# Kernel tuning notes

Hardware: AMD Instinct MI355X
Metric: run time of the kernel (lower is better)

The kernel has to match this reference:

```python
import jax, jax.numpy as jnp
import numpy as np

N_EMBED = 384
HEAD_SIZE = 64
B, T = 512, 256


def setup_inputs() -> dict:
    key = jax.random.key(0)
    kx, kq, kk, kv = jax.random.split(key, 4)
    x = jax.random.normal(kx, (B, T, N_EMBED), dtype=jnp.float32)
    # nn.Linear(n_embed, head_size, bias=False): y = x @ W^T with W [head_size, n_embed].
    # We store the transposed [n_embed, head_size] matrices directly.
    s = 1.0 / np.sqrt(N_EMBED)
    Wq = jax.random.uniform(kq, (N_EMBED, HEAD_SIZE), jnp.float32, -s, s)
    Wk = jax.random.uniform(kk, (N_EMBED, HEAD_SIZE), jnp.float32, -s, s)
    Wv = jax.random.uniform(kv, (N_EMBED, HEAD_SIZE), jnp.float32, -s, s)
    return {"x": x, "Wq": Wq, "Wk": Wk, "Wv": Wv}


def reference(x, Wq, Wk, Wv):
    # Single-head causal self-attention (dropout in eval mode = identity).
    q = jnp.einsum("btc,cd->btd", x, Wq)  # [B,T,D]
    k = jnp.einsum("btc,cd->btd", x, Wk)
    v = jnp.einsum("btc,cd->btd", x, Wv)
    scale = jnp.asarray(k.shape[-1], x.dtype) ** -0.5
    wei = jnp.einsum("btd,bsd->bts", q, k) * scale  # [B,T,T]
    t = wei.shape[-1]
    causal = jnp.tril(jnp.ones((t, t), dtype=bool))
    wei = jnp.where(causal, wei, -jnp.inf)
    wei = jax.nn.softmax(wei, axis=-1)
    out = jnp.einsum("bts,bsd->btd", wei, v)  # [B,T,D]
    return out
```

## Files before the change

kernel.cpp:

```cpp
#include <hip/hip_runtime.h>

#define BATCH 512
#define SEQ   256
#define CEMB  384
#define HD    64
#define MROWS (BATCH*SEQ)

typedef __bf16 bf16_t;
typedef __bf16 bf16x4 __attribute__((ext_vector_type(4)));
typedef __bf16 bf16x8 __attribute__((ext_vector_type(8)));
typedef float  f32x4  __attribute__((ext_vector_type(4)));

#define GLOAD_LDS16(gp, lp) \
    __builtin_amdgcn_global_load_lds((const __attribute__((address_space(1))) void*)(gp), \
                                     (__attribute__((address_space(3))) void*)(lp), 16, 0, 0)

__global__ void wconv_kernel(const float* __restrict__ Wq, const float* __restrict__ Wk,
                             const float* __restrict__ Wv, bf16_t* __restrict__ Wf) {
    int idx = blockIdx.x * 256 + threadIdx.x;
    if (idx >= 144 * 512) return;
    int j = idx & 7, lane = (idx >> 3) & 63, f = idx >> 9;
    int ni = f % 12, s = f / 12;
    int n = ni * 16 + (lane & 15);
    int k = s * 32 + ((lane >> 4) << 3) + j;
    const float* W = (n < 64) ? Wq : ((n < 128) ? Wk : Wv);
    Wf[idx] = (bf16_t)W[k * HD + (n & 63)];
}

__device__ inline bf16x8 cvt8(float4 a, float4 b) {
    bf16x8 r;
    r[0] = (bf16_t)a.x; r[1] = (bf16_t)a.y; r[2] = (bf16_t)a.z; r[3] = (bf16_t)a.w;
    r[4] = (bf16_t)b.x; r[5] = (bf16_t)b.y; r[6] = (bf16_t)b.z; r[7] = (bf16_t)b.w;
    return r;
}

__global__ __launch_bounds__(512, 2)
void qkv_kernel(const float* __restrict__ x, const bf16_t* __restrict__ Wf,
                bf16_t* __restrict__ qg, bf16_t* __restrict__ kg, bf16_t* __restrict__ vg) {
    __shared__ char smem[147456];

    const int tid = threadIdx.x;
    const int w = tid >> 6, lane = tid & 63;
    const int l15 = lane & 15, l4 = lane >> 4;

    #pragma unroll
    for (int i = 0; i < 18; ++i)
        GLOAD_LDS16((const char*)Wf + tid * 16 + i * 8192, smem + tid * 16 + i * 8192);
    __syncthreads();

    const char* wp = smem + lane * 16;

    #pragma unroll
    for (int u = 0; u < 2; ++u) {
        const long rowbase = (long)blockIdx.x * 256 + (u * 8 + w) * 16;
        const float* aptr = x + (rowbase + l15) * CEMB + l4 * 8;

        f32x4 acc[12];
        #pragma unroll
        for (int ni = 0; ni < 12; ++ni) acc[ni] = f32x4{0.f, 0.f, 0.f, 0.f};

        #pragma unroll
        for (int hf = 0; hf < 2; ++hf) {
            float4 A[6][2];
            #pragma unroll
            for (int s = 0; s < 6; ++s) {
                A[s][0] = *(const float4*)(aptr + (hf * 6 + s) * 32);
                A[s][1] = *(const float4*)(aptr + (hf * 6 + s) * 32 + 4);
            }
            #pragma unroll
            for (int s = 0; s < 6; ++s) {
                bf16x8 af = cvt8(A[s][0], A[s][1]);
                const int ks = hf * 6 + s;
                #pragma unroll
                for (int ni = 0; ni < 12; ++ni) {
                    bf16x8 bf = *(const bf16x8*)(wp + (ks * 12 + ni) * 1024);
                    acc[ni] = __builtin_amdgcn_mfma_f32_16x16x32_bf16(af, bf, acc[ni], 0, 0, 0);
                }
            }
        }

        #pragma unroll
        for (int ni = 0; ni < 12; ++ni) {
            int col = ni * 16 + l15;
            bf16_t* dst = (col < 64) ? qg : ((col < 128) ? kg : vg);
            int d = col & 63;
            #pragma unroll
            for (int r = 0; r < 4; ++r) {
                long rg = rowbase + l4 * 4 + r;
                dst[rg * HD + d] = (bf16_t)acc[ni][r];
            }
        }
    }
}

__global__ __launch_bounds__(256, 2)
void attn_kernel(const bf16_t* __restrict__ qg, const bf16_t* __restrict__ kg,
                 const bf16_t* __restrict__ vg, float* __restrict__ out) {
    __shared__ char smem[81920];

    const int tid = threadIdx.x;
    const int w = tid >> 6, lane = tid & 63;
    const int l15 = lane & 15, l4 = lane >> 4;
    const long base = (long)blockIdx.x * SEQ * HD;

    for (int it = 0; it < 8; ++it) {
        int i = tid + it * 256;
        int s = i >> 3, cb = (i & 7) * 16;
        bf16x8 kv = *(const bf16x8*)(kg + base + (long)i * 8);
        *(bf16x8*)(smem + s * 128 + (cb ^ ((s & 7) << 4))) = kv;
    }
    for (int it = 0; it < 8; ++it) {
        int i = tid + it * 256;
        int s = i >> 3, d0 = (i & 7) * 8;
        bf16x8 vv = *(const bf16x8*)(vg + base + (long)i * 8);
        #pragma unroll
        for (int j = 0; j < 8; ++j) {
            int d = d0 + j;
            *(bf16_t*)(smem + 32768 + d * 512 + ((s * 2) ^ ((d & 7) << 4))) = vv[j];
        }
    }

    bf16x8 qf[4][2];
    #pragma unroll
    for (int mi = 0; mi < 4; ++mi) {
        int row = mi * 64 + w * 16 + l15;
        #pragma unroll
        for (int kk = 0; kk < 2; ++kk)
            qf[mi][kk] = *(const bf16x8*)(qg + base + (long)row * HD + kk * 32 + l4 * 8);
    }

    __syncthreads();

    f32x4 oacc[4][4];
    float mrow[4][4], lrow[4][4];
    #pragma unroll
    for (int mi = 0; mi < 4; ++mi) {
        #pragma unroll
        for (int di = 0; di < 4; ++di) oacc[mi][di] = f32x4{0.f, 0.f, 0.f, 0.f};
        #pragma unroll
        for (int r = 0; r < 4; ++r) { mrow[mi][r] = -1e30f; lrow[mi][r] = 0.f; }
    }

    char* Pw = smem + 65536 + w * 4096;
    const int ntiles = (w < 2) ? 7 : 8;
    const float LOG2E = 1.44269504089f;

    for (int st = 0; st < ntiles; ++st) {
        f32x4 sacc[4][2];
        #pragma unroll
        for (int mi = 0; mi < 4; ++mi)
            #pragma unroll
            for (int ni = 0; ni < 2; ++ni) sacc[mi][ni] = f32x4{0.f, 0.f, 0.f, 0.f};

        #pragma unroll
        for (int kk = 0; kk < 2; ++kk) {
            #pragma unroll
            for (int ni = 0; ni < 2; ++ni) {
                int s = st * 32 + ni * 16 + l15;
                bf16x8 kf = *(const bf16x8*)(smem + s * 128 + (((kk * 32 + l4 * 8) * 2) ^ ((s & 7) << 4)));
                #pragma unroll
                for (int mi = 0; mi < 4; ++mi) {
                    if (st * 32 <= mi * 64 + w * 16 + 15)
                        sacc[mi][ni] = __builtin_amdgcn_mfma_f32_16x16x32_bf16(qf[mi][kk], kf, sacc[mi][ni], 0, 0, 0);
                }
            }
        }

        #pragma unroll
        for (int mi = 0; mi < 4; ++mi) {
            const int R = mi * 64 + w * 16;
            if (st * 32 > R + 15) continue;
            const bool needmask = (st * 32 + 31 > R);
            #pragma unroll
            for (int r = 0; r < 4; ++r) {
                float s0 = sacc[mi][0][r] * 0.125f;
                float s1 = sacc[mi][1][r] * 0.125f;
                if (needmask) {
                    int row = R + l4 * 4 + r;
                    if (st * 32 + l15 > row)      s0 = -1e30f;
                    if (st * 32 + 16 + l15 > row) s1 = -1e30f;
                }
                float mx = fmaxf(s0, s1);
                mx = fmaxf(mx, __shfl_xor(mx, 1));
                mx = fmaxf(mx, __shfl_xor(mx, 2));
                mx = fmaxf(mx, __shfl_xor(mx, 4));
                mx = fmaxf(mx, __shfl_xor(mx, 8));
                float mold = mrow[mi][r];
                float mnew = fmaxf(mold, mx);
                float alpha = exp2f((mold - mnew) * LOG2E);
                float p0 = exp2f((s0 - mnew) * LOG2E);
                float p1 = exp2f((s1 - mnew) * LOG2E);
                mrow[mi][r] = mnew;
                float rs = p0 + p1;
                rs += __shfl_xor(rs, 1);
                rs += __shfl_xor(rs, 2);
                rs += __shfl_xor(rs, 4);
                rs += __shfl_xor(rs, 8);
                lrow[mi][r] = lrow[mi][r] * alpha + rs;
                #pragma unroll
                for (int di = 0; di < 4; ++di) oacc[mi][di][r] *= alpha;
                int q = mi * 16 + l4 * 4 + r;
                *(bf16_t*)(Pw + q * 64 + ((l15 * 2) ^ ((q & 3) << 4))) = (bf16_t)p0;
                *(bf16_t*)(Pw + q * 64 + ((32 + l15 * 2) ^ ((q & 3) << 4))) = (bf16_t)p1;
            }
        }

        #pragma unroll
        for (int mi = 0; mi < 4; ++mi) {
            if (st * 32 > mi * 64 + w * 16 + 15) continue;
            int q = mi * 16 + l15;
            bf16x8 pf = *(const bf16x8*)(Pw + q * 64 + ((l4 * 16) ^ ((q & 3) << 4)));
            #pragma unroll
            for (int di = 0; di < 4; ++di) {
                int d = di * 16 + l15;
                bf16x8 vf = *(const bf16x8*)(smem + 32768 + d * 512 + (((st * 32 + l4 * 8) * 2) ^ ((d & 7) << 4)));
                oacc[mi][di] = __builtin_amdgcn_mfma_f32_16x16x32_bf16(pf, vf, oacc[mi][di], 0, 0, 0);
            }
        }
    }

    #pragma unroll
    for (int mi = 0; mi < 4; ++mi) {
        #pragma unroll
        for (int r = 0; r < 4; ++r) {
            float inv = 1.f / lrow[mi][r];
            long row = mi * 64 + w * 16 + l4 * 4 + r;
            #pragma unroll
            for (int di = 0; di < 4; ++di)
                out[base + row * HD + di * 16 + l15] = oacc[mi][di][r] * inv;
        }
    }
}

extern "C" void kernel_launch(void* const* d_in, const int* in_sizes, int n_in,
                              void* d_out, int out_size, void* d_ws, size_t ws_size,
                              hipStream_t stream) {
    const float* x  = (const float*)d_in[0];
    const float* Wq = (const float*)d_in[1];
    const float* Wk = (const float*)d_in[2];
    const float* Wv = (const float*)d_in[3];
    float* out = (float*)d_out;

    bf16_t* Wf = (bf16_t*)d_ws;
    bf16_t* qg = (bf16_t*)((char*)d_ws + (1 << 20));
    bf16_t* kg = qg + (long)MROWS * HD;
    bf16_t* vg = kg + (long)MROWS * HD;

    wconv_kernel<<<dim3(288), dim3(256), 0, stream>>>(Wq, Wk, Wv, Wf);
    qkv_kernel<<<dim3(512), dim3(512), 0, stream>>>(x, Wf, qg, kg, vg);
    attn_kernel<<<dim3(BATCH), dim3(256), 0, stream>>>(qg, kg, vg, out);
}
```

Baseline: 104.3 us.

## Retile QKV projection: stage converted x tile in LDS, double-buffer weight slices

The QKV projection kernel now stages a 128-row slice of x, converted to bf16, in padded LDS. It streams weight k-slices through a double-buffered LDS ring instead of loading the full 144KB weight matrix per block. Each wave computes a 64x48 output tile (4x3 MFMA fragments), so fragments are reused in registers and A rows are no longer reloaded per wave. The grid doubles to 1024 blocks. This adds a barrier per k-step and an upfront serial x load with no overlap against compute.

```diff
diff --git a/kernel.cpp b/kernel.cpp
--- a/kernel.cpp
+++ b/kernel.cpp
@@ -6,8 +6,10 @@
 #define HD    64
 #define MROWS (BATCH*SEQ)
 
+#define ABYTES 100352
+#define BBYTES 12288
+
 typedef __bf16 bf16_t;
-typedef __bf16 bf16x4 __attribute__((ext_vector_type(4)));
 typedef __bf16 bf16x8 __attribute__((ext_vector_type(8)));
 typedef float  f32x4  __attribute__((ext_vector_type(4)));
 
@@ -37,57 +39,79 @@
 __global__ __launch_bounds__(512, 2)
 void qkv_kernel(const float* __restrict__ x, const bf16_t* __restrict__ Wf,
                 bf16_t* __restrict__ qg, bf16_t* __restrict__ kg, bf16_t* __restrict__ vg) {
-    __shared__ char smem[147456];
+    __shared__ char smem[ABYTES + 2 * BBYTES];
 
     const int tid = threadIdx.x;
     const int w = tid >> 6, lane = tid & 63;
     const int l15 = lane & 15, l4 = lane >> 4;
-
-    #pragma unroll
-    for (int i = 0; i < 18; ++i)
-        GLOAD_LDS16((const char*)Wf + tid * 16 + i * 8192, smem + tid * 16 + i * 8192);
+    const int rg = w >> 2, cs = w & 3;
+    const long blockrow = (long)blockIdx.x * 128;
+
+    #pragma unroll
+    for (int half = 0; half < 2; ++half) {
+        float4 ar[6][2];
+        #pragma unroll
+        for (int i = 0; i < 6; ++i) {
+            int c = tid + (half * 6 + i) * 512;
+            const float* src = x + (blockrow + c / 48) * CEMB + (c % 48) * 8;
+            ar[i][0] = *(const float4*)src;
+            ar[i][1] = *(const float4*)(src + 4);
+        }
+        #pragma unroll
+        for (int i = 0; i < 6; ++i) {
+            int c = tid + (half * 6 + i) * 512;
+            *(bf16x8*)(smem + (c / 48) * 784 + (c % 48) * 16) = cvt8(ar[i][0], ar[i][1]);
+        }
+    }
+
+    GLOAD_LDS16((const char*)Wf + tid * 16, smem + ABYTES + tid * 16);
+    if (tid < 256)
+        GLOAD_LDS16((const char*)Wf + (512 + tid) * 16, smem + ABYTES + (512 + tid) * 16);
     __syncthreads();
 
-    const char* wp = smem + lane * 16;
-
-    #pragma unroll
-    for (int u = 0; u < 2; ++u) {
-        const long rowbase = (long)blockIdx.x * 256 + (u * 8 + w) * 16;
-        const float* aptr = x + (rowbase + l15) * CEMB + l4 * 8;
-
-        f32x4 acc[12];
-        #pragma unroll
-        for (int ni = 0; ni < 12; ++ni) acc[ni] = f32x4{0.f, 0.f, 0.f, 0.f};
-
-        #pragma unroll
-        for (int hf = 0; hf < 2; ++hf) {
-            float4 A[6][2];
-            #pragma unroll
-            for (int s = 0; s < 6; ++s) {
-                A[s][0] = *(const float4*)(aptr + (hf * 6 + s) * 32);
-                A[s][1] = *(const float4*)(aptr + (hf * 6 + s) * 32 + 4);
-            }
-            #pragma unroll
-            for (int s = 0; s < 6; ++s) {
-                bf16x8 af = cvt8(A[s][0], A[s][1]);
-                const int ks = hf * 6 + s;
-                #pragma unroll
-                for (int ni = 0; ni < 12; ++ni) {
-                    bf16x8 bf = *(const bf16x8*)(wp + (ks * 12 + ni) * 1024);
-                    acc[ni] = __builtin_amdgcn_mfma_f32_16x16x32_bf16(af, bf, acc[ni], 0, 0, 0);
-                }
-            }
-        }
-
-        #pragma unroll
-        for (int ni = 0; ni < 12; ++ni) {
-            int col = ni * 16 + l15;
+    f32x4 acc[4][3];
+    #pragma unroll
+    for (int rf = 0; rf < 4; ++rf)
+        #pragma unroll
+        for (int nj = 0; nj < 3; ++nj) acc[rf][nj] = f32x4{0.f, 0.f, 0.f, 0.f};
+
+    for (int ks = 0; ks < 12; ++ks) {
+        const int cur = ks & 1, nxt = cur ^ 1;
+        if (ks < 11) {
+            const char* bsrc = (const char*)Wf + (ks + 1) * BBYTES;
+            char* bdst = smem + ABYTES + nxt * BBYTES;
+            GLOAD_LDS16(bsrc + tid * 16, bdst + tid * 16);
+            if (tid < 256)
+                GLOAD_LDS16(bsrc + (512 + tid) * 16, bdst + (512 + tid) * 16);
+        }
+
+        bf16x8 bfrag[3];
+        #pragma unroll
+        for (int nj = 0; nj < 3; ++nj)
+            bfrag[nj] = *(const bf16x8*)(smem + ABYTES + cur * BBYTES +
+                                         (cs * 3 + nj) * 1024 + lane * 16);
+        #pragma unroll
+        for (int rf = 0; rf < 4; ++rf) {
+            bf16x8 af = *(const bf16x8*)(smem + (rg * 64 + rf * 16 + l15) * 784 +
+                                         ks * 64 + l4 * 16);
+            #pragma unroll
+            for (int nj = 0; nj < 3; ++nj)
+                acc[rf][nj] = __builtin_amdgcn_mfma_f32_16x16x32_bf16(af, bfrag[nj], acc[rf][nj], 0, 0, 0);
+        }
+        __syncthreads();
+    }
+
+    #pragma unroll
+    for (int rf = 0; rf < 4; ++rf) {
+        #pragma unroll
+        for (int nj = 0; nj < 3; ++nj) {
+            int col = cs * 48 + nj * 16 + l15;
             bf16_t* dst = (col < 64) ? qg : ((col < 128) ? kg : vg);
             int d = col & 63;
             #pragma unroll
             for (int r = 0; r < 4; ++r) {
-                long rg = rowbase + l4 * 4 + r;
-                dst[rg * HD + d] = (bf16_t)acc[ni][r];
+                long row = blockrow + rg * 64 + rf * 16 + l4 * 4 + r;
+                dst[row * HD + d] = (bf16_t)acc[rf][nj][r];
             }
         }
     }
@@ -247,6 +271,6 @@
     bf16_t* vg = kg + (long)MROWS * HD;
 
     wconv_kernel<<<dim3(288), dim3(256), 0, stream>>>(Wq, Wk, Wv, Wf);
-    qkv_kernel<<<dim3(512), dim3(512), 0, stream>>>(x, Wf, qg, kg, vg);
+    qkv_kernel<<<dim3(MROWS / 128), dim3(512), 0, stream>>>(x, Wf, qg, kg, vg);
     attn_kernel<<<dim3(BATCH), dim3(256), 0, stream>>>(qg, kg, vg, out);
 }
```

After: 109.4 us. 4.9% more time.

## Restructure QKV projection into small tiles with LDS-staged x and double-buffered weights

Applied to the files above, without the earlier changes.

The QKV projection kernel now gives each block a 32-row tile instead of 256 rows, launching 4096 blocks of 256 threads. The full fp32 x tile is staged into LDS with an XOR swizzle via async global-to-LDS loads. Weight k-slices are streamed through a double buffer rather than preloading all 144KB of weights per block. The intent is to cut the large per-block LDS footprint and weight preload so more blocks can be resident and latency is better hidden, at the cost of a barrier per k-step and weights being re-read by many more blocks.

```diff
diff --git a/kernel.cpp b/kernel.cpp
--- a/kernel.cpp
+++ b/kernel.cpp
@@ -6,8 +6,10 @@
 #define HD    64
 #define MROWS (BATCH*SEQ)
 
+#define ABYTES 49152
+#define BBYTES 12288
+
 typedef __bf16 bf16_t;
-typedef __bf16 bf16x4 __attribute__((ext_vector_type(4)));
 typedef __bf16 bf16x8 __attribute__((ext_vector_type(8)));
 typedef float  f32x4  __attribute__((ext_vector_type(4)));
 
@@ -34,61 +36,71 @@
     return r;
 }
 
-__global__ __launch_bounds__(512, 2)
+__global__ __launch_bounds__(256, 2)
 void qkv_kernel(const float* __restrict__ x, const bf16_t* __restrict__ Wf,
                 bf16_t* __restrict__ qg, bf16_t* __restrict__ kg, bf16_t* __restrict__ vg) {
-    __shared__ char smem[147456];
+    __shared__ char smem[ABYTES + 2 * BBYTES];
 
     const int tid = threadIdx.x;
     const int w = tid >> 6, lane = tid & 63;
     const int l15 = lane & 15, l4 = lane >> 4;
-
-    #pragma unroll
-    for (int i = 0; i < 18; ++i)
-        GLOAD_LDS16((const char*)Wf + tid * 16 + i * 8192, smem + tid * 16 + i * 8192);
+    const int rf = w >> 1, ch = w & 1;
+    const long blockrow = (long)blockIdx.x * 32;
+    const char* xb = (const char*)x + blockrow * (CEMB * 4);
+
+    #pragma unroll
+    for (int i = 0; i < 12; ++i) {
+        int c = i * 256 + tid;
+        int row = c / 96, q = (c % 96) * 16;
+        GLOAD_LDS16(xb + row * 1536 + (q ^ ((row & 7) << 4)), smem + c * 16);
+    }
+    #pragma unroll
+    for (int i = 0; i < 3; ++i) {
+        int c = i * 256 + tid;
+        GLOAD_LDS16((const char*)Wf + c * 16, smem + ABYTES + c * 16);
+    }
     __syncthreads();
 
-    const char* wp = smem + lane * 16;
-
-    #pragma unroll
-    for (int u = 0; u < 2; ++u) {
-        const long rowbase = (long)blockIdx.x * 256 + (u * 8 + w) * 16;
-        const float* aptr = x + (rowbase + l15) * CEMB + l4 * 8;
-
-        f32x4 acc[12];
-        #pragma unroll
-        for (int ni = 0; ni < 12; ++ni) acc[ni] = f32x4{0.f, 0.f, 0.f, 0.f};
-
-        #pragma unroll
-        for (int hf = 0; hf < 2; ++hf) {
-            float4 A[6][2];
-            #pragma unroll
-            for (int s = 0; s < 6; ++s) {
-                A[s][0] = *(const float4*)(aptr + (hf * 6 + s) * 32);
-                A[s][1] = *(const float4*)(aptr + (hf * 6 + s) * 32 + 4);
-            }
-            #pragma unroll
-            for (int s = 0; s < 6; ++s) {
-                bf16x8 af = cvt8(A[s][0], A[s][1]);
-                const int ks = hf * 6 + s;
-                #pragma unroll
-                for (int ni = 0; ni < 12; ++ni) {
-                    bf16x8 bf = *(const bf16x8*)(wp + (ks * 12 + ni) * 1024);
-                    acc[ni] = __builtin_amdgcn_mfma_f32_16x16x32_bf16(af, bf, acc[ni], 0, 0, 0);
-                }
-            }
-        }
-
-        #pragma unroll
-        for (int ni = 0; ni < 12; ++ni) {
-            int col = ni * 16 + l15;
-            bf16_t* dst = (col < 64) ? qg : ((col < 128) ? kg : vg);
-            int d = col & 63;
-            #pragma unroll
-            for (int r = 0; r < 4; ++r) {
-                long rg = rowbase + l4 * 4 + r;
-                dst[rg * HD + d] = (bf16_t)acc[ni][r];
-            }
+    f32x4 acc[6];
+    #pragma unroll
+    for (int nj = 0; nj < 6; ++nj) acc[nj] = f32x4{0.f, 0.f, 0.f, 0.f};
+
+    for (int ks = 0; ks < 12; ++ks) {
+        const int cur = ks & 1, nxt = cur ^ 1;
+        if (ks < 11) {
+            #pragma unroll
+            for (int i = 0; i < 3; ++i) {
+                int c = i * 256 + tid;
+                GLOAD_LDS16((const char*)Wf + (ks + 1) * BBYTES + c * 16,
+                            smem + ABYTES + nxt * BBYTES + c * 16);
+            }
+        }
+
+        const int rowl = rf * 16 + l15;
+        const int boff = ks * 128 + l4 * 32;
+        const int swz = (l15 & 7) << 4;
+        float4 f0 = *(const float4*)(smem + rowl * 1536 + (boff ^ swz));
+        float4 f1 = *(const float4*)(smem + rowl * 1536 + ((boff + 16) ^ swz));
+        bf16x8 af = cvt8(f0, f1);
+
+        #pragma unroll
+        for (int nj = 0; nj < 6; ++nj) {
+            bf16x8 bf = *(const bf16x8*)(smem + ABYTES + cur * BBYTES +
+                                         (ch * 6 + nj) * 1024 + lane * 16);
+            acc[nj] = __builtin_amdgcn_mfma_f32_16x16x32_bf16(af, bf, acc[nj], 0, 0, 0);
+        }
+        __syncthreads();
+    }
+
+    #pragma unroll
+    for (int nj = 0; nj < 6; ++nj) {
+        int col = (ch * 6 + nj) * 16 + l15;
+        bf16_t* dst = (col < 64) ? qg : ((col < 128) ? kg : vg);
+        int d = col & 63;
+        #pragma unroll
+        for (int r = 0; r < 4; ++r) {
+            long row = blockrow + rf * 16 + l4 * 4 + r;
+            dst[row * HD + d] = (bf16_t)acc[nj][r];
         }
     }
 }
@@ -247,6 +259,6 @@
     bf16_t* vg = kg + (long)MROWS * HD;
 
     wconv_kernel<<<dim3(288), dim3(256), 0, stream>>>(Wq, Wk, Wv, Wf);
-    qkv_kernel<<<dim3(512), dim3(512), 0, stream>>>(x, Wf, qg, kg, vg);
+    qkv_kernel<<<dim3(MROWS / 32), dim3(256), 0, stream>>>(x, Wf, qg, kg, vg);
     attn_kernel<<<dim3(BATCH), dim3(256), 0, stream>>>(qg, kg, vg, out);
 }
```

Measured after the change: 131.8 us. 1.26x slower.
